# Kernel optimization log

Measured on AMD Instinct MI355X. Metric: run time of the kernel, lower is better.

Reference implementation:

```python
import jax, jax.numpy as jnp
import numpy as np

HIDDEN = 128
VEL_SCALE = 0.5
T_END = 1.0


def conv1x1(x, w, b):
    # x: [B, Cin, N], w: [Cout, Cin], b: [Cout]
    return jnp.einsum('oi,bin->bon', w, x) + b[None, :, None]


def setup_inputs() -> dict:
    key = jax.random.key(0)
    ks = jax.random.split(key, 11)
    B, N = 8, 50000
    def winit(k, shape, fan_in):
        bound = 1.0 / np.sqrt(fan_in)
        return jax.random.uniform(k, shape, jnp.float32, -bound, bound)
    return {
        'x0': jax.random.normal(ks[0], (B, 3, N), jnp.float32),
        'h1_w': winit(ks[1], (HIDDEN, 4), 4), 'h1_b': winit(ks[2], (HIDDEN,), 4),
        'g1_w': winit(ks[3], (HIDDEN, 4), 4), 'g1_b': winit(ks[4], (HIDDEN,), 4),
        'h2_w': winit(ks[5], (HIDDEN, HIDDEN), HIDDEN), 'h2_b': winit(ks[6], (HIDDEN,), HIDDEN),
        'g2_w': winit(ks[7], (HIDDEN, HIDDEN), HIDDEN), 'g2_b': winit(ks[8], (HIDDEN,), HIDDEN),
        'out_w': winit(ks[9], (3, HIDDEN), HIDDEN), 'out_b': winit(ks[10], (3,), HIDDEN),
    }


def field(t, x, h1_w, h1_b, g1_w, g1_b, h2_w, h2_b, g2_w, g2_b, out_w, out_b):
    B, _, N = x.shape
    t_chan = jnp.broadcast_to(jnp.reshape(t, (1, 1, 1)), (B, 1, N))
    z = jnp.concatenate([x, t_chan], axis=1)                 # [B, 4, N]
    z = conv1x1(z, h1_w, h1_b) * jax.nn.sigmoid(conv1x1(z, g1_w, g1_b))
    z = jax.nn.relu(z)
    z = conv1x1(z, h2_w, h2_b) * jax.nn.sigmoid(conv1x1(z, g2_w, g2_b))
    z = jax.nn.relu(z)
    v = conv1x1(z, out_w, out_b)                             # [B, 3, N]
    return jnp.tanh(v) * VEL_SCALE


def reference(x0, h1_w, h1_b, g1_w, g1_b, h2_w, h2_b, g2_w, g2_b, out_w, out_b):
    params = (h1_w, h1_b, g1_w, g1_b, h2_w, h2_b, g2_w, g2_b, out_w, out_b)
    f = lambda t, y: field(jnp.asarray(t, jnp.float32), y, *params)
    # torchdiffeq 'rk4' with t=[0, T] and no step_size: single 3/8-rule RK4 step, h = T
    h = jnp.float32(T_END)
    t0 = jnp.float32(0.0)
    third = jnp.float32(1.0 / 3.0)
    k1 = f(t0, x0)
    k2 = f(t0 + h * third, x0 + h * k1 * third)
    k3 = f(t0 + h * third * 2.0, x0 + h * (k2 - k1 * third))
    k4 = f(t0 + h, x0 + h * (k1 - k2 + k3))
    return x0 + h * (k1 + 3.0 * (k2 + k3) + k4) * jnp.float32(0.125)
```

## Files before the change

### kernel.cpp

```cpp
#include <hip/hip_runtime.h>
#include <math.h>
#include <utility>

typedef __attribute__((ext_vector_type(8))) short    bf16x8;
typedef __attribute__((ext_vector_type(4))) float    f32x4;
typedef __attribute__((ext_vector_type(2))) float    f32x2;
typedef __attribute__((ext_vector_type(2))) unsigned u32x2;
typedef __attribute__((ext_vector_type(4))) unsigned u32x4;

template<int I, int N, class F>
__device__ __forceinline__ void sfor(F&& f) {
    if constexpr (I < N) { f(std::integral_constant<int, I>{}); sfor<I + 1, N>(static_cast<F&&>(f)); }
}

#define NPT    50000
#define NBLK   3125
#define Z_S    128
#define LOG2E  1.4426950408889634f

#define OFF_Z1   0
#define OFF_Z2   32768
#define OFF_ZIN  65536
#define OFF_AOW  67584
#define OFF_BIAS 68352
#define OFF_A1   70464
#define LDS_BYTES 72512
#define TBZ   8192
#define TBZIN 512

static __device__ __forceinline__ unsigned packbf(float a, float b) {
    unsigned r;
    asm("v_cvt_pk_bf16_f32 %0, %1, %2" : "=v"(r) : "v"(a), "v"(b));
    return r;
}

#if defined(__has_builtin)
#if __has_builtin(__builtin_amdgcn_exp2f) && __has_builtin(__builtin_amdgcn_rcpf)
#define HAVE_RAW_TRANS 1
#endif
#endif

#ifdef HAVE_RAW_TRANS
static __device__ __forceinline__ float fexp2(float x) { return __builtin_amdgcn_exp2f(x); }
static __device__ __forceinline__ float frcp(float x)  { return __builtin_amdgcn_rcpf(x); }
#else
static __device__ __forceinline__ float fexp2(float x) { return __exp2f(x); }
static __device__ __forceinline__ float frcp(float x)  { return __frcp_rn(x); }
#endif

static __device__ __forceinline__ unsigned gate2p(f32x2 h, f32x2 gp) {
    f32x2 e;
    e.x = fexp2(gp.x);
    e.y = fexp2(gp.y);
    f32x2 p = e + 1.f;
    float ip = frcp(p.x * p.y);
    f32x2 ps = __builtin_shufflevector(p, p, 1, 0);
    f32x2 z = (h * ps) * ip;
    z = __builtin_elementwise_max(z, f32x2{0.f, 0.f});
    return packbf(z.x, z.y);
}

static __device__ __forceinline__ bf16x8 pack8s(const float* p, float s) {
    f32x4 lo = *reinterpret_cast<const f32x4*>(p);
    f32x4 hi = *reinterpret_cast<const f32x4*>(p + 4);
    u32x4 u = { packbf(lo[0]*s, lo[1]*s), packbf(lo[2]*s, lo[3]*s),
                packbf(hi[0]*s, hi[1]*s), packbf(hi[2]*s, hi[3]*s) };
    return __builtin_bit_cast(bf16x8, u);
}
static __device__ __forceinline__ f32x4 mfma16(bf16x8 a, bf16x8 b, f32x4 c) {
    return __builtin_amdgcn_mfma_f32_16x16x32_bf16(a, b, c, 0, 0, 0);
}

__global__ __launch_bounds__(512, 4) void node_rk4_mfma(
    const float* __restrict__ x0,
    const float* __restrict__ h1_w, const float* __restrict__ h1_b,
    const float* __restrict__ g1_w, const float* __restrict__ g1_b,
    const float* __restrict__ h2_w, const float* __restrict__ h2_b,
    const float* __restrict__ g2_w, const float* __restrict__ g2_b,
    const float* __restrict__ out_w, const float* __restrict__ out_b,
    float* __restrict__ y)
{
    extern __shared__ char lds_raw[];
    short*    z1s    = reinterpret_cast<short*>(lds_raw + OFF_Z1);
    short*    z2s    = reinterpret_cast<short*>(lds_raw + OFF_Z2);
    short*    zin    = reinterpret_cast<short*>(lds_raw + OFF_ZIN);
    short*    aow_s  = reinterpret_cast<short*>(lds_raw + OFF_AOW);
    float*    bias_s = reinterpret_cast<float*>(lds_raw + OFF_BIAS);
    unsigned* a1_s   = reinterpret_cast<unsigned*>(lds_raw + OFF_A1);

    const int tid  = threadIdx.x;
    const int w    = tid >> 6;
    const int lane = tid & 63;
    const int q    = lane >> 4;
    const int m    = lane & 15;

    const int row = 16 * w + m;
    bf16x8 a2h[4], a2g[4];
    sfor<0, 4>([&](auto KS) {
        constexpr int ks = KS.value;
        a2h[ks] = pack8s(h2_w + row * 128 + ks * 32 + q * 8, 1.0f);
        a2g[ks] = pack8s(g2_w + row * 128 + ks * 32 + q * 8, -LOG2E);
    });
    if (tid < 128) {
        const f32x4 t1 = *reinterpret_cast<const f32x4*>(h1_w + tid * 4);
        const f32x4 t2 = *reinterpret_cast<const f32x4*>(g1_w + tid * 4);
        a1_s[tid * 2]           = packbf(t1[0], t1[1]);
        a1_s[tid * 2 + 1]       = packbf(t1[2], t1[3]);
        a1_s[256 + tid * 2]     = packbf(t2[0] * -LOG2E, t2[1] * -LOG2E);
        a1_s[256 + tid * 2 + 1] = packbf(t2[2] * -LOG2E, t2[3] * -LOG2E);
    }
    if (w == 0 && m < 3) {
        sfor<0, 4>([&](auto KS) {
            constexpr int ks = KS.value;
            bf16x8 t = pack8s(out_w + m * 128 + ks * 32 + q * 8, 2.f * LOG2E);
            *reinterpret_cast<bf16x8*>(&aow_s[((ks * 3 + m) * 4 + q) * 8]) = t;
        });
    }
    if (tid < 128) {
        bias_s[tid]       = h1_b[tid];
        bias_s[128 + tid] = g1_b[tid] * -LOG2E;
        bias_s[256 + tid] = h2_b[tid];
        bias_s[384 + tid] = g2_b[tid] * -LOG2E;
    }
    if (tid < 16) bias_s[512 + tid] = (tid < 3) ? out_b[tid] * (2.f * LOG2E) : 0.f;

    if (tid < 128) *reinterpret_cast<u32x4*>(&zin[tid * 8]) = u32x4{0u, 0u, 0u, 0u};

    const float third = 1.0f / 3.0f;
    const int cb4 = 16 * w + 4 * q;

    const int m7   = m & 7;
    const int qx8  = (q ^ (m & 3)) * 8;
    const int m4_8 = (m & 4) * 8;

    const short* zin_rd = &zin[m * 8];
    short*       zin_wr = &zin[row * 8];
    const short* z1_re  = &z1s[m * Z_S + qx8 + m4_8];
    const short* z1_ro  = &z1s[m * Z_S + qx8 + (m4_8 ^ 32)];
    short*       z1_wr  = &z1s[m * Z_S + (((2 * w + (q >> 1)) ^ m7) * 8) + (q & 1) * 4];
    short*       z2_wr  = &z2s[m * Z_S + (((2 * w + (q >> 1)) ^ m7) * 8) + (q & 1) * 4];
    const short* z2_re  = &z2s[row * Z_S + qx8 + m4_8];
    const short* z2_ro  = &z2s[row * Z_S + qx8 + (m4_8 ^ 32)];
    const float* bs     = &bias_s[cb4];
    const float* bsov   = &bias_s[512 + 4 * q];

    float xc0 = 0.f, xc1 = 0.f, xc2 = 0.f;
    int gbase = 0;
    if (lane < 16) {
        const int pg = blockIdx.x * 128 + row;
        const int bb = pg / NPT;
        gbase = bb * 3 * NPT + (pg - bb * NPT);
        xc0 = x0[gbase]; xc1 = x0[gbase + NPT]; xc2 = x0[gbase + 2 * NPT];
    }
    float ax = 0.f, ay = 0.f, az = 0.f;
    float k1x = 0.f, k1y = 0.f, k1z = 0.f, k2x = 0.f, k2y = 0.f, k2z = 0.f;

    __syncthreads();

    bf16x8 a1h = {0,0,0,0,0,0,0,0}, a1g = {0,0,0,0,0,0,0,0};
    if (q == 0) {
        u32x2 th = *reinterpret_cast<const u32x2*>(&a1_s[row * 2]);
        u32x2 tg = *reinterpret_cast<const u32x2*>(&a1_s[256 + row * 2]);
        u32x4 uh = { th[0], th[1], 0u, 0u };
        u32x4 ug = { tg[0], tg[1], 0u, 0u };
        a1h = __builtin_bit_cast(bf16x8, uh);
        a1g = __builtin_bit_cast(bf16x8, ug);
    }
    bf16x8 aow[4];
    {
        const short* aow_rd = &aow_s[((m < 3 ? m : 2) * 4 + q) * 8];
        sfor<0, 4>([&](auto KS) {
            constexpr int ks = KS.value;
            aow[ks] = *reinterpret_cast<const bf16x8*>(aow_rd + ks * 96);
        });
    }

    if (lane < 16) {
        u32x2 pk = { packbf(xc0, xc1), packbf(xc2, 0.f) };
        *reinterpret_cast<u32x2*>(zin_wr) = pk;
    }
    __syncthreads();

    #pragma unroll 1
    for (int s = 0; s < 4; ++s) {
        {
            const f32x4 b1h = *reinterpret_cast<const f32x4*>(bs);
            const f32x4 b1g = *reinterpret_cast<const f32x4*>(bs + 128);
            sfor<0, 2>([&](auto TT) {
                constexpr int T = TT.value;
                sfor<0, 4>([&](auto NT) {
                    constexpr int nt = NT.value;
                    bf16x8 bf = *reinterpret_cast<const bf16x8*>(zin_rd + T * TBZIN + nt * 128);
                    f32x4 ch = mfma16(a1h, bf, b1h);
                    f32x4 cg = mfma16(a1g, bf, b1g);
                    u32x2 pk = { gate2p(f32x2{ch[0], ch[1]}, f32x2{cg[0], cg[1]}),
                                 gate2p(f32x2{ch[2], ch[3]}, f32x2{cg[2], cg[3]}) };
                    *reinterpret_cast<u32x2*>(z1_wr + T * TBZ + nt * 2048) = pk;
                });
            });
        }
        __syncthreads();

        {
            const f32x4 b2h = *reinterpret_cast<const f32x4*>(bs + 256);
            const f32x4 b2g = *reinterpret_cast<const f32x4*>(bs + 384);
            sfor<0, 2>([&](auto TT) {
                constexpr int T = TT.value;
                sfor<0, 2>([&](auto NTP) {
                    constexpr int b0 = T * TBZ + (2 * NTP.value) * 2048;
                    constexpr int b1 = T * TBZ + (2 * NTP.value + 1) * 2048;
                    f32x4 c0h, c1h, c0g, c1g;
                    {
                        bf16x8 f0 = *reinterpret_cast<const bf16x8*>(z1_re + b0);
                        bf16x8 f1 = *reinterpret_cast<const bf16x8*>(z1_re + b1);
                        c0h = mfma16(a2h[0], f0, b2h); c1h = mfma16(a2h[0], f1, b2h);
                        c0g = mfma16(a2g[0], f0, b2g); c1g = mfma16(a2g[0], f1, b2g);
                    }
                    sfor<1, 4>([&](auto KS) {
                        constexpr int ks = KS.value;
                        const short* zb = (ks & 1) ? z1_ro : z1_re;
                        constexpr int koff = (ks & 2) ? 64 : 0;
                        bf16x8 f0 = *reinterpret_cast<const bf16x8*>(zb + b0 + koff);
                        bf16x8 f1 = *reinterpret_cast<const bf16x8*>(zb + b1 + koff);
                        c0h = mfma16(a2h[ks], f0, c0h); c1h = mfma16(a2h[ks], f1, c1h);
                        c0g = mfma16(a2g[ks], f0, c0g); c1g = mfma16(a2g[ks], f1, c1g);
                    });
                    u32x2 pk0 = { gate2p(f32x2{c0h[0], c0h[1]}, f32x2{c0g[0], c0g[1]}),
                                  gate2p(f32x2{c0h[2], c0h[3]}, f32x2{c0g[2], c0g[3]}) };
                    *reinterpret_cast<u32x2*>(z2_wr + b0) = pk0;
                    u32x2 pk1 = { gate2p(f32x2{c1h[0], c1h[1]}, f32x2{c1g[0], c1g[1]}),
                                  gate2p(f32x2{c1h[2], c1h[3]}, f32x2{c1g[2], c1g[3]}) };
                    *reinterpret_cast<u32x2*>(z2_wr + b1) = pk1;
                });
            });
        }
        __syncthreads();

        {
            f32x4 vc = *reinterpret_cast<const f32x4*>(bsov);
            sfor<0, 4>([&](auto KS) {
                constexpr int ks = KS.value;
                const short* zb = (ks & 1) ? z2_ro : z2_re;
                constexpr int koff = (ks & 2) ? 64 : 0;
                bf16x8 bf = *reinterpret_cast<const bf16x8*>(zb + koff);
                vc = mfma16(aow[ks], bf, vc);
            });
            f32x2 e; e.x = fexp2(vc[0]); e.y = fexp2(vc[1]);
            f32x2 p = e + 1.f;
            const float ipxy = frcp(p.x * p.y);
            const float kx = 0.5f - p.y * ipxy;
            const float ky = 0.5f - p.x * ipxy;
            const float kz = 0.5f - frcp(fexp2(vc[2]) + 1.f);

            if (lane < 16) {
                float zi0, zi1, zi2, tt;
                bool do_stage = true;
                if (s == 0) {
                    ax = kx; ay = ky; az = kz;
                    k1x = kx; k1y = ky; k1z = kz;
                    zi0 = fmaf(kx, third, xc0);
                    zi1 = fmaf(ky, third, xc1);
                    zi2 = fmaf(kz, third, xc2); tt = third;
                } else if (s == 1) {
                    ax = fmaf(3.f, kx, ax); ay = fmaf(3.f, ky, ay); az = fmaf(3.f, kz, az);
                    k2x = kx; k2y = ky; k2z = kz;
                    zi0 = xc0 + (kx - k1x * third);
                    zi1 = xc1 + (ky - k1y * third);
                    zi2 = xc2 + (kz - k1z * third); tt = 2.f * third;
                } else if (s == 2) {
                    ax = fmaf(3.f, kx, ax); ay = fmaf(3.f, ky, ay); az = fmaf(3.f, kz, az);
                    zi0 = xc0 + (k1x - k2x + kx);
                    zi1 = xc1 + (k1y - k2y + ky);
                    zi2 = xc2 + (k1z - k2z + kz); tt = 1.f;
                } else {
                    ax += kx; ay += ky; az += kz;
                    do_stage = false; zi0 = zi1 = zi2 = tt = 0.f;
                }
                if (do_stage) {
                    u32x2 pk = { packbf(zi0, zi1), packbf(zi2, tt) };
                    *reinterpret_cast<u32x2*>(zin_wr) = pk;
                }
            }
        }
        if (s < 3) __syncthreads();
    }

    if (lane < 16) {
        y[gbase]           = fmaf(0.125f, ax, xc0);
        y[gbase + NPT]     = fmaf(0.125f, ay, xc1);
        y[gbase + 2 * NPT] = fmaf(0.125f, az, xc2);
    }
}

extern "C" void kernel_launch(void* const* d_in, const int* in_sizes, int n_in,
                              void* d_out, int out_size, void* d_ws, size_t ws_size,
                              hipStream_t stream) {
    (void)in_sizes; (void)n_in; (void)d_ws; (void)ws_size; (void)out_size;
    const float* x0    = (const float*)d_in[0];
    const float* h1_w  = (const float*)d_in[1];
    const float* h1_b  = (const float*)d_in[2];
    const float* g1_w  = (const float*)d_in[3];
    const float* g1_b  = (const float*)d_in[4];
    const float* h2_w  = (const float*)d_in[5];
    const float* h2_b  = (const float*)d_in[6];
    const float* g2_w  = (const float*)d_in[7];
    const float* g2_b  = (const float*)d_in[8];
    const float* out_w = (const float*)d_in[9];
    const float* out_b = (const float*)d_in[10];
    float* y = (float*)d_out;

    static bool attr_set = false;
    if (!attr_set) {
        (void)hipFuncSetAttribute(reinterpret_cast<const void*>(&node_rk4_mfma),
                                  hipFuncAttributeMaxDynamicSharedMemorySize, LDS_BYTES);
        attr_set = true;
    }
    node_rk4_mfma<<<NBLK, 512, LDS_BYTES, stream>>>(
        x0, h1_w, h1_b, g1_w, g1_b, h2_w, h2_b, g2_w, g2_b, out_w, out_b, y);
}
```

Baseline: 241.8 us.

## Fuse output head and first layer per wave, removing zin staging barrier

```diff
diff --git a/kernel.cpp b/kernel.cpp
--- a/kernel.cpp
+++ b/kernel.cpp
@@ -20,13 +20,11 @@
 
 #define OFF_Z1   0
 #define OFF_Z2   32768
-#define OFF_ZIN  65536
-#define OFF_AOW  67584
-#define OFF_BIAS 68352
-#define OFF_A1   70464
-#define LDS_BYTES 72512
+#define OFF_AOW  65536
+#define OFF_BIAS 66304
+#define OFF_A1   68416
+#define LDS_BYTES 70464
 #define TBZ   8192
-#define TBZIN 512
 
 static __device__ __forceinline__ unsigned packbf(float a, float b) {
     unsigned r;
@@ -83,7 +81,6 @@
     extern __shared__ char lds_raw[];
     short*    z1s    = reinterpret_cast<short*>(lds_raw + OFF_Z1);
     short*    z2s    = reinterpret_cast<short*>(lds_raw + OFF_Z2);
-    short*    zin    = reinterpret_cast<short*>(lds_raw + OFF_ZIN);
     short*    aow_s  = reinterpret_cast<short*>(lds_raw + OFF_AOW);
     float*    bias_s = reinterpret_cast<float*>(lds_raw + OFF_BIAS);
     unsigned* a1_s   = reinterpret_cast<unsigned*>(lds_raw + OFF_A1);
@@ -124,24 +121,23 @@
     }
     if (tid < 16) bias_s[512 + tid] = (tid < 3) ? out_b[tid] * (2.f * LOG2E) : 0.f;
 
-    if (tid < 128) *reinterpret_cast<u32x4*>(&zin[tid * 8]) = u32x4{0u, 0u, 0u, 0u};
-
     const float third = 1.0f / 3.0f;
     const int cb4 = 16 * w + 4 * q;
 
     const int m7   = m & 7;
     const int qx8  = (q ^ (m & 3)) * 8;
     const int m4_8 = (m & 4) * 8;
-
-    const short* zin_rd = &zin[m * 8];
-    short*       zin_wr = &zin[row * 8];
+    const int qh   = q >> 1;
+    const int ql4  = (q & 1) * 4;
+
     const short* z1_re  = &z1s[m * Z_S + qx8 + m4_8];
     const short* z1_ro  = &z1s[m * Z_S + qx8 + (m4_8 ^ 32)];
-    short*       z1_wr  = &z1s[m * Z_S + (((2 * w + (q >> 1)) ^ m7) * 8) + (q & 1) * 4];
-    short*       z2_wr  = &z2s[m * Z_S + (((2 * w + (q >> 1)) ^ m7) * 8) + (q & 1) * 4];
+    short*       z2_wr  = &z2s[m * Z_S + (((2 * w + qh) ^ m7) * 8) + ql4];
     const short* z2_re  = &z2s[row * Z_S + qx8 + m4_8];
     const short* z2_ro  = &z2s[row * Z_S + qx8 + (m4_8 ^ 32)];
+    short*       z1f_wr = &z1s[row * Z_S + ql4];
     const float* bs     = &bias_s[cb4];
+    const float* bsq    = &bias_s[4 * q];
     const float* bsov   = &bias_s[512 + 4 * q];
 
     float xc0 = 0.f, xc1 = 0.f, xc2 = 0.f;
@@ -157,15 +153,6 @@
 
     __syncthreads();
 
-    bf16x8 a1h = {0,0,0,0,0,0,0,0}, a1g = {0,0,0,0,0,0,0,0};
-    if (q == 0) {
-        u32x2 th = *reinterpret_cast<const u32x2*>(&a1_s[row * 2]);
-        u32x2 tg = *reinterpret_cast<const u32x2*>(&a1_s[256 + row * 2]);
-        u32x4 uh = { th[0], th[1], 0u, 0u };
-        u32x4 ug = { tg[0], tg[1], 0u, 0u };
-        a1h = __builtin_bit_cast(bf16x8, uh);
-        a1g = __builtin_bit_cast(bf16x8, ug);
-    }
     bf16x8 aow[4];
     {
         const short* aow_rd = &aow_s[((m < 3 ? m : 2) * 4 + q) * 8];
@@ -175,29 +162,75 @@
         });
     }
 
-    if (lane < 16) {
-        u32x2 pk = { packbf(xc0, xc1), packbf(xc2, 0.f) };
-        *reinterpret_cast<u32x2*>(zin_wr) = pk;
-    }
-    __syncthreads();
+    auto L1F = [&](float zi0, float zi1, float zi2, float tt) {
+        bf16x8 bin = {0, 0, 0, 0, 0, 0, 0, 0};
+        if (q == 0) {
+            u32x4 ub = { packbf(zi0, zi1), packbf(zi2, tt), 0u, 0u };
+            bin = __builtin_bit_cast(bf16x8, ub);
+        }
+        sfor<0, 8>([&](auto G) {
+            constexpr int g = G.value;
+            bf16x8 ah = {0,0,0,0,0,0,0,0}, ag = {0,0,0,0,0,0,0,0};
+            if (q == 0) {
+                u32x2 th = *reinterpret_cast<const u32x2*>(&a1_s[(16 * g + m) * 2]);
+                u32x2 tg = *reinterpret_cast<const u32x2*>(&a1_s[256 + (16 * g + m) * 2]);
+                u32x4 uh = { th[0], th[1], 0u, 0u };
+                u32x4 ug = { tg[0], tg[1], 0u, 0u };
+                ah = __builtin_bit_cast(bf16x8, uh);
+                ag = __builtin_bit_cast(bf16x8, ug);
+            }
+            const f32x4 b1h = *reinterpret_cast<const f32x4*>(bsq + 16 * g);
+            const f32x4 b1g = *reinterpret_cast<const f32x4*>(bsq + 128 + 16 * g);
+            f32x4 ch = mfma16(ah, bin, b1h);
+            f32x4 cg = mfma16(ag, bin, b1g);
+            u32x2 pk = { gate2p(f32x2{ch[0], ch[1]}, f32x2{cg[0], cg[1]}),
+                         gate2p(f32x2{ch[2], ch[3]}, f32x2{cg[2], cg[3]}) };
+            *reinterpret_cast<u32x2*>(z1f_wr + (((2 * g + qh) ^ m7) * 8)) = pk;
+        });
+    };
 
     #pragma unroll 1
     for (int s = 0; s < 4; ++s) {
-        {
-            const f32x4 b1h = *reinterpret_cast<const f32x4*>(bs);
-            const f32x4 b1g = *reinterpret_cast<const f32x4*>(bs + 128);
-            sfor<0, 2>([&](auto TT) {
-                constexpr int T = TT.value;
-                sfor<0, 4>([&](auto NT) {
-                    constexpr int nt = NT.value;
-                    bf16x8 bf = *reinterpret_cast<const bf16x8*>(zin_rd + T * TBZIN + nt * 128);
-                    f32x4 ch = mfma16(a1h, bf, b1h);
-                    f32x4 cg = mfma16(a1g, bf, b1g);
-                    u32x2 pk = { gate2p(f32x2{ch[0], ch[1]}, f32x2{cg[0], cg[1]}),
-                                 gate2p(f32x2{ch[2], ch[3]}, f32x2{cg[2], cg[3]}) };
-                    *reinterpret_cast<u32x2*>(z1_wr + T * TBZ + nt * 2048) = pk;
-                });
+        if (s > 0) {
+            f32x4 vc = *reinterpret_cast<const f32x4*>(bsov);
+            sfor<0, 4>([&](auto KS) {
+                constexpr int ks = KS.value;
+                const short* zb = (ks & 1) ? z2_ro : z2_re;
+                constexpr int koff = (ks & 2) ? 64 : 0;
+                bf16x8 bf = *reinterpret_cast<const bf16x8*>(zb + koff);
+                vc = mfma16(aow[ks], bf, vc);
             });
+            f32x2 e; e.x = fexp2(vc[0]); e.y = fexp2(vc[1]);
+            f32x2 p = e + 1.f;
+            const float ipxy = frcp(p.x * p.y);
+            const float kx = 0.5f - p.y * ipxy;
+            const float ky = 0.5f - p.x * ipxy;
+            const float kz = 0.5f - frcp(fexp2(vc[2]) + 1.f);
+
+            float zi0 = 0.f, zi1 = 0.f, zi2 = 0.f, tt = 0.f;
+            if (lane < 16) {
+                if (s == 1) {
+                    ax = kx; ay = ky; az = kz;
+                    k1x = kx; k1y = ky; k1z = kz;
+                    zi0 = fmaf(kx, third, xc0);
+                    zi1 = fmaf(ky, third, xc1);
+                    zi2 = fmaf(kz, third, xc2); tt = third;
+                } else if (s == 2) {
+                    ax = fmaf(3.f, kx, ax); ay = fmaf(3.f, ky, ay); az = fmaf(3.f, kz, az);
+                    k2x = kx; k2y = ky; k2z = kz;
+                    zi0 = xc0 + (kx - k1x * third);
+                    zi1 = xc1 + (ky - k1y * third);
+                    zi2 = xc2 + (kz - k1z * third); tt = 2.f * third;
+                } else {
+                    ax = fmaf(3.f, kx, ax); ay = fmaf(3.f, ky, ay); az = fmaf(3.f, kz, az);
+                    zi0 = xc0 + (k1x - k2x + kx);
+                    zi1 = xc1 + (k1y - k2y + ky);
+                    zi2 = xc2 + (k1z - k2z + kz); tt = 1.f;
+                }
+            }
+            L1F(zi0, zi1, zi2, tt);
+        } else {
+            L1F(xc0, xc1, xc2, 0.f);
         }
         __syncthreads();
 
@@ -235,60 +268,30 @@
             });
         }
         __syncthreads();
-
-        {
-            f32x4 vc = *reinterpret_cast<const f32x4*>(bsov);
-            sfor<0, 4>([&](auto KS) {
-                constexpr int ks = KS.value;
-                const short* zb = (ks & 1) ? z2_ro : z2_re;
-                constexpr int koff = (ks & 2) ? 64 : 0;
-                bf16x8 bf = *reinterpret_cast<const bf16x8*>(zb + koff);
-                vc = mfma16(aow[ks], bf, vc);
-            });
-            f32x2 e; e.x = fexp2(vc[0]); e.y = fexp2(vc[1]);
-            f32x2 p = e + 1.f;
-            const float ipxy = frcp(p.x * p.y);
-            const float kx = 0.5f - p.y * ipxy;
-            const float ky = 0.5f - p.x * ipxy;
-            const float kz = 0.5f - frcp(fexp2(vc[2]) + 1.f);
-
-            if (lane < 16) {
-                float zi0, zi1, zi2, tt;
-                bool do_stage = true;
-                if (s == 0) {
-                    ax = kx; ay = ky; az = kz;
-                    k1x = kx; k1y = ky; k1z = kz;
-                    zi0 = fmaf(kx, third, xc0);
-                    zi1 = fmaf(ky, third, xc1);
-                    zi2 = fmaf(kz, third, xc2); tt = third;
-                } else if (s == 1) {
-                    ax = fmaf(3.f, kx, ax); ay = fmaf(3.f, ky, ay); az = fmaf(3.f, kz, az);
-                    k2x = kx; k2y = ky; k2z = kz;
-                    zi0 = xc0 + (kx - k1x * third);
-                    zi1 = xc1 + (ky - k1y * third);
-                    zi2 = xc2 + (kz - k1z * third); tt = 2.f * third;
-                } else if (s == 2) {
-                    ax = fmaf(3.f, kx, ax); ay = fmaf(3.f, ky, ay); az = fmaf(3.f, kz, az);
-                    zi0 = xc0 + (k1x - k2x + kx);
-                    zi1 = xc1 + (k1y - k2y + ky);
-                    zi2 = xc2 + (k1z - k2z + kz); tt = 1.f;
-                } else {
-                    ax += kx; ay += ky; az += kz;
-                    do_stage = false; zi0 = zi1 = zi2 = tt = 0.f;
-                }
-                if (do_stage) {
-                    u32x2 pk = { packbf(zi0, zi1), packbf(zi2, tt) };
-                    *reinterpret_cast<u32x2*>(zin_wr) = pk;
-                }
-            }
+    }
+
+    {
+        f32x4 vc = *reinterpret_cast<const f32x4*>(bsov);
+        sfor<0, 4>([&](auto KS) {
+            constexpr int ks = KS.value;
+            const short* zb = (ks & 1) ? z2_ro : z2_re;
+            constexpr int koff = (ks & 2) ? 64 : 0;
+            bf16x8 bf = *reinterpret_cast<const bf16x8*>(zb + koff);
+            vc = mfma16(aow[ks], bf, vc);
+        });
+        f32x2 e; e.x = fexp2(vc[0]); e.y = fexp2(vc[1]);
+        f32x2 p = e + 1.f;
+        const float ipxy = frcp(p.x * p.y);
+        const float kx = 0.5f - p.y * ipxy;
+        const float ky = 0.5f - p.x * ipxy;
+        const float kz = 0.5f - frcp(fexp2(vc[2]) + 1.f);
+
+        if (lane < 16) {
+            ax += kx; ay += ky; az += kz;
+            y[gbase]           = fmaf(0.125f, ax, xc0);
+            y[gbase + NPT]     = fmaf(0.125f, ay, xc1);
+            y[gbase + 2 * NPT] = fmaf(0.125f, az, xc2);
         }
-        if (s < 3) __syncthreads();
-    }
-
-    if (lane < 16) {
-        y[gbase]           = fmaf(0.125f, ax, xc0);
-        y[gbase + NPT]     = fmaf(0.125f, ay, xc1);
-        y[gbase + 2 * NPT] = fmaf(0.125f, az, xc2);
     }
 }
 
```

New measurement: 257.5 us. 6.5% more time.
